# Performance work log

Measured on AMD Instinct MI355X. Metric: run time of the kernel, lower is better.

The kernel has to match this reference:

```python
import jax, jax.numpy as jnp
import numpy as np
import math

B, S, D = 4, 2048, 1024
NH = 8
DH = D // NH
EPS = 1e-6


def setup_inputs() -> dict:
    key = jax.random.key(0)
    k0, k1, k2, k3, k4, k5 = jax.random.split(key, 6)
    q = jax.random.normal(k0, (B, S, D), jnp.float32)
    k = jax.random.normal(k1, (B, S, D), jnp.float32)
    v = jax.random.normal(k2, (B, S, D), jnp.float32)
    # Gate Dense params. Original inits kernels to zeros; use small random
    # kernels so gates actually depend on the input.
    W_i = jax.random.normal(k3, (3 * D, NH), jnp.float32) * 0.02
    b_i = jax.random.normal(k4, (NH,), jnp.float32) * 0.1
    W_f = jax.random.normal(k5, (3 * D, NH), jnp.float32) * 0.02
    b_f = jnp.linspace(3.0, 6.0, NH, dtype=jnp.float32)  # bias_linspace_init(3,6)
    ln_w = jnp.ones((NH, DH), jnp.float32)  # MultiHeadLayerNorm weight (no bias)
    c_state = jnp.zeros((B, NH, DH, DH), jnp.float32)
    n_state = jnp.zeros((B, NH, DH, 1), jnp.float32)
    m_state = jnp.zeros((B, NH, 1, 1), jnp.float32)
    return {"q": q, "k": k, "v": v, "c_state": c_state, "n_state": n_state,
            "m_state": m_state, "W_i": W_i, "b_i": b_i, "W_f": W_f,
            "b_f": b_f, "ln_w": ln_w}


def _mlstm_forward(q, k, v, c_state, n_state, m_state, W_i, b_i, W_f, b_f, ln_w):
    Bq, Sq, Dq = q.shape
    nh = b_i.shape[0]
    dh = Dq // nh
    scale = 1.0 / math.sqrt(dh)

    qkv = jnp.concatenate([q, k, v], axis=-1)            # (B,S,3D)
    ig = (qkv @ W_i + b_i).transpose(0, 2, 1)            # (B,NH,S)
    fg = (qkv @ W_f + b_f).transpose(0, 2, 1)            # (B,NH,S)

    # Faithful 'weaving' reshape (no head transpose!)
    qh = q.reshape(Bq, nh, Sq, dh)
    kh = k.reshape(Bq, nh, Sq, dh)
    vh = v.reshape(Bq, nh, Sq, dh)

    # scan layout: time-major
    qs = qh.transpose(2, 0, 1, 3)                        # (S,B,NH,DH)
    ks_ = kh.transpose(2, 0, 1, 3)
    vs = vh.transpose(2, 0, 1, 3)
    igs = ig.transpose(2, 0, 1)[:, :, :, None, None]     # (S,B,NH,1,1)
    fgs = fg.transpose(2, 0, 1)[:, :, :, None, None]

    def step(carry, xs):
        c, n, m = carry
        qt, kt, vt, ft, it = xs
        qt = qt[:, :, None, :]                           # (B,NH,1,DH)
        kt = kt[..., None]                               # (B,NH,DH,1)
        vt = vt[:, :, None, :]                           # (B,NH,1,DH)
        log_f = jax.nn.log_sigmoid(ft)                   # (B,NH,1,1)
        m_new = jnp.maximum(log_f + m, it)
        f_act = jnp.exp(log_f + m - m_new)
        i_act = jnp.exp(it - m_new)
        k_sc = kt * scale
        c_new = f_act * c + i_act * (k_sc @ vt)          # (B,NH,DH,DH)
        n_new = f_act * n + i_act * k_sc                 # (B,NH,DH,1)
        h_num = qt @ c_new                               # (B,NH,1,DH)
        qn = qt @ n_new                                  # (B,NH,1,1)
        denom = jnp.maximum(jnp.abs(qn), jnp.exp(-m_new)) + EPS
        h = (h_num / denom).squeeze(axis=2)              # (B,NH,DH)
        return (c_new, n_new, m_new), h

    (c_f, n_f, m_f), out = jax.lax.scan(
        step, (c_state, n_state, m_state), (qs, ks_, vs, fgs, igs))
    h = out.transpose(1, 2, 0, 3)                        # (B,NH,S,DH)

    # MultiHeadLayerNorm over DH, per-head scale, no bias
    mu = h.mean(axis=-1, keepdims=True)
    var = h.var(axis=-1, keepdims=True)
    hn = (h - mu) * jax.lax.rsqrt(var + 1e-6) * ln_w[None, :, None, :]
    hn = hn.transpose(0, 2, 1, 3).reshape(Bq, Sq, Dq)
    return hn, c_f, n_f, m_f


def reference(q, k, v, c_state, n_state, m_state, W_i, b_i, W_f, b_f, ln_w):
    return _mlstm_forward(q, k, v, c_state, n_state, m_state,
                          W_i, b_i, W_f, b_f, ln_w)
```

## Files before the change

### kernel.cpp

```cpp
#include <hip/hip_runtime.h>
#include <math.h>

#define BB 4
#define SS 2048
#define DD 1024
#define NHD 8
#define DHD 128
#define NC 16
#define CL 128
#define SCALE 0.08838834764831845f

#define OFF_IG   0
#define OFF_LF   65536
#define OFF_B    131072
#define OFF_G    196608
#define OFF_E    262144
#define OFF_RM   327680
#define OFF_MIN  393216
#define OFF_SC   393728
#define OFF_UN   396288
#define OFF_NIN  461824
#define OFF_U    527360
#define OFF_KH   4721664
#define OFF_VT   8915968
#define OUT_C  8388608
#define OUT_N  8912896
#define OUT_M  8916992

typedef __attribute__((ext_vector_type(8))) _Float16 f16x8;
typedef __attribute__((ext_vector_type(4))) float f32x4;

__device__ __forceinline__ unsigned pk2h(float a, float b) {
  union { _Float16 h[2]; unsigned u; } f;
  f.h[0] = (_Float16)a; f.h[1] = (_Float16)b;
  return f.u;
}
__device__ __forceinline__ f16x8 mkfrag(float4 a, float4 c) {
  f16x8 f;
  f[0] = (_Float16)a.x; f[1] = (_Float16)a.y; f[2] = (_Float16)a.z; f[3] = (_Float16)a.w;
  f[4] = (_Float16)c.x; f[5] = (_Float16)c.y; f[6] = (_Float16)c.z; f[7] = (_Float16)c.w;
  return f;
}
__device__ __forceinline__ char* swp(char* base, int row, int byte) {
  return base + (((row << 8) + byte) ^ ((row & 7) << 4));
}

__global__ __launch_bounds__(256) void wtrans_kernel(const float* __restrict__ Wi,
                                                     const float* __restrict__ Wf,
                                                     _Float16* __restrict__ WT) {
  const int kk = blockIdx.x * 256 + threadIdx.x;
  float4 wa = *(const float4*)(Wi + (size_t)kk * 8);
  float4 wb = *(const float4*)(Wi + (size_t)kk * 8 + 4);
  float4 fa = *(const float4*)(Wf + (size_t)kk * 8);
  float4 fb = *(const float4*)(Wf + (size_t)kk * 8 + 4);
  WT[0 * 3072 + kk]  = (_Float16)wa.x; WT[1 * 3072 + kk]  = (_Float16)wa.y;
  WT[2 * 3072 + kk]  = (_Float16)wa.z; WT[3 * 3072 + kk]  = (_Float16)wa.w;
  WT[4 * 3072 + kk]  = (_Float16)wb.x; WT[5 * 3072 + kk]  = (_Float16)wb.y;
  WT[6 * 3072 + kk]  = (_Float16)wb.z; WT[7 * 3072 + kk]  = (_Float16)wb.w;
  WT[8 * 3072 + kk]  = (_Float16)fa.x; WT[9 * 3072 + kk]  = (_Float16)fa.y;
  WT[10 * 3072 + kk] = (_Float16)fa.z; WT[11 * 3072 + kk] = (_Float16)fa.w;
  WT[12 * 3072 + kk] = (_Float16)fb.x; WT[13 * 3072 + kk] = (_Float16)fb.y;
  WT[14 * 3072 + kk] = (_Float16)fb.z; WT[15 * 3072 + kk] = (_Float16)fb.w;
}

__global__ __launch_bounds__(512) void gates_kernel(
    const float* __restrict__ q, const float* __restrict__ k, const float* __restrict__ v,
    const _Float16* __restrict__ WT, const float* __restrict__ bi,
    const float* __restrict__ bfb,
    float* __restrict__ ig_ws, float* __restrict__ lf_ws,
    _Float16* __restrict__ kh) {
  __shared__ float red[8][256];
  const int tid = threadIdx.x, wid = tid >> 6, lane = tid & 63;
  const int g16 = lane >> 4, l15 = lane & 15;
  const int g0 = blockIdx.x * 16;
  const int b = g0 >> 11, t0 = g0 & (SS - 1);

  const size_t rowoff = (size_t)b * SS * DD + (size_t)(t0 + l15) * DD;
  const float* qr = q + rowoff;
  const float* kr = k + rowoff;
  const float* vr = v + rowoff;

  f32x4 acc = {0.f, 0.f, 0.f, 0.f};
  const int ks0 = wid * 12;
  #pragma unroll
  for (int grp = 0; grp < 3; ++grp) {
    const int s0 = ks0 + grp * 4;
    const int seg = s0 >> 5;
    const float* base = (seg == 0) ? qr : (seg == 1) ? kr : vr;
    const float* Ab = base + (s0 & 31) * 32 + g16 * 8;
    const _Float16* Bb = WT + l15 * 3072 + s0 * 32 + g16 * 8;
    float4 a[4], c[4]; f16x8 bfr[4];
    #pragma unroll
    for (int j = 0; j < 4; ++j) {
      a[j]   = *(const float4*)(Ab + j * 32);
      c[j]   = *(const float4*)(Ab + j * 32 + 4);
      bfr[j] = *(const f16x8*)(Bb + j * 32);
    }
    if (seg == 1) {
      const int coff = (s0 & 31) * 32 + g16 * 8;
      #pragma unroll
      for (int j = 0; j < 4; ++j)
        *(f16x8*)(kh + rowoff + coff + j * 32) = mkfrag(a[j], c[j]);
    }
    #pragma unroll
    for (int j = 0; j < 4; ++j)
      acc = __builtin_amdgcn_mfma_f32_16x16x32_f16(mkfrag(a[j], c[j]), bfr[j], acc, 0, 0, 0);
  }
  #pragma unroll
  for (int r = 0; r < 4; ++r) red[wid][(g16 * 4 + r) * 16 + l15] = acc[r];
  __syncthreads();

  if (tid < 256) {
    float s = 0.f;
    #pragma unroll
    for (int w = 0; w < 8; ++w) s += red[w][tid];
    const int row = tid >> 4, gate = tid & 15;
    const int t = t0 + row;
    if (gate < 8) {
      ig_ws[(size_t)(b * NHD + gate) * SS + t] = s + bi[gate];
    } else {
      float ft = s + bfb[gate - 8];
      float lf = fminf(ft, 0.f) - log1pf(expf(-fabsf(ft)));
      lf_ws[(size_t)(b * NHD + gate - 8) * SS + t] = lf;
    }
  }
}

__global__ __launch_bounds__(128) void prep1_kernel(float* __restrict__ ws) {
  const int g  = blockIdx.x & 15;
  const int bh = blockIdx.x >> 4;
  const int s  = threadIdx.x;
  __shared__ float sh[128];
  __shared__ float bc1;
  const int t = g * CL + s;
  float lfv = ws[OFF_LF + (size_t)bh * SS + t];
  float iv  = ws[OFF_IG + (size_t)bh * SS + t];
  float v = lfv;
  sh[s] = v; __syncthreads();
  for (int off = 1; off < 128; off <<= 1) {
    float tv = (s >= off) ? sh[s - off] : 0.f;
    __syncthreads();
    v += tv; sh[s] = v; __syncthreads();
  }
  float Bv = v;
  float Gv = iv - Bv;
  v = Gv; sh[s] = v; __syncthreads();
  for (int off = 1; off < 128; off <<= 1) {
    float tv = (s >= off) ? sh[s - off] : -3.0e38f;
    __syncthreads();
    v = fmaxf(v, tv); sh[s] = v; __syncthreads();
  }
  float Rv = v;
  if (s == 127) bc1 = Rv;
  __syncthreads();
  float mxG = bc1;
  ws[OFF_B  + (size_t)bh * SS + t] = Bv;
  ws[OFF_G  + (size_t)bh * SS + t] = Gv;
  ws[OFF_RM + (size_t)bh * SS + t] = Rv;
  ws[OFF_E  + (size_t)bh * SS + t] = expf(Gv - mxG);
}

__global__ __launch_bounds__(64) void prep2_kernel(float* __restrict__ ws,
                                                   const float* __restrict__ m0,
                                                   float* __restrict__ out) {
  const int bh = blockIdx.x;
  if (threadIdx.x != 0) return;
  const float m0v = m0[bh];
  float m_run = m0v, LFtot = 0.f;
  float mina[NC], mxga[NC], lfsa[NC];
  #pragma unroll
  for (int g = 0; g < NC; ++g) {
    float Bend = ws[OFF_B  + (size_t)bh * SS + g * CL + 127];
    float mxG  = ws[OFF_RM + (size_t)bh * SS + g * CL + 127];
    ws[OFF_MIN + bh * NC + g] = m_run;
    mina[g] = m_run; mxga[g] = mxG; lfsa[g] = LFtot;
    m_run = Bend + fmaxf(m_run, mxG);
    LFtot += Bend;
  }
  out[OUT_M + bh] = m_run;
  float* sc = ws + OFF_SC + bh * 80;
  float S = -3.0e38f;
  #pragma unroll
  for (int g = 0; g < NC; ++g) {
    float r_g = lfsa[g] - mina[g];
    sc[g]      = expf(S + r_g);
    sc[20 + g] = expf(m0v + lfsa[g] - mina[g]);
    float s_g = mxga[g] - lfsa[g];
    float Sn = fmaxf(S, s_g);
    sc[40 + g] = expf(S - Sn);
    sc[60 + g] = expf(s_g - Sn);
    S = Sn;
  }
  sc[16] = expf(S + LFtot - m_run);
  sc[36] = expf(m0v + LFtot - m_run);
}

__global__ __launch_bounds__(256, 2) void u_kernel(const float* __restrict__ k,
                                                   const float* __restrict__ v,
                                                   float* __restrict__ ws) {
  extern __shared__ char smem[];
  char* Kt = smem;
  char* Vt = smem + 32768;

  const int tid = threadIdx.x;
  const int wid = tid >> 6;
  const int lane = tid & 63;
  const int g16 = lane >> 4;
  const int l15 = lane & 15;
  const int g  = blockIdx.x & 15;
  const int bh = blockIdx.x >> 4;
  const int b = bh >> 3, hh = bh & 7;
  const size_t headoff = (size_t)b * SS * DD + (size_t)hh * SS * DHD;
  const float* kb = k + headoff + (size_t)g * CL * DHD;
  const float* vb = v + headoff + (size_t)g * CL * DHD;
  const float* E  = ws + OFF_E + (size_t)bh * SS + g * CL;

  #pragma unroll 4
  for (int it = 0; it < 16; ++it) {
    const int idx = (it << 8) + tid;
    const int c  = idx & 127;
    const int r0 = (idx >> 7) << 2;
    float e0 = E[r0] * SCALE, e1 = E[r0 + 1] * SCALE,
          e2 = E[r0 + 2] * SCALE, e3 = E[r0 + 3] * SCALE;
    float a0 = kb[(size_t)r0 * DHD + c] * e0;
    float a1 = kb[(size_t)(r0 + 1) * DHD + c] * e1;
    float a2 = kb[(size_t)(r0 + 2) * DHD + c] * e2;
    float a3 = kb[(size_t)(r0 + 3) * DHD + c] * e3;
    *(uint2*)swp(Kt, c, r0 * 2) = make_uint2(pk2h(a0, a1), pk2h(a2, a3));
    float b0 = vb[(size_t)r0 * DHD + c];
    float b1 = vb[(size_t)(r0 + 1) * DHD + c];
    float b2 = vb[(size_t)(r0 + 2) * DHD + c];
    float b3 = vb[(size_t)(r0 + 3) * DHD + c];
    *(uint2*)swp(Vt, c, r0 * 2) = make_uint2(pk2h(b0, b1), pk2h(b2, b3));
  }
  __syncthreads();

  _Float16* VTg = (_Float16*)(ws + OFF_VT) + (size_t)(bh * NC + g) * 16384;
  #pragma unroll
  for (int it2 = 0; it2 < 8; ++it2) {
    const int ci = (it2 << 8) + tid;
    const int j = ci >> 4, rp = ci & 15;
    f16x8 x = *(f16x8*)swp(Vt, j, rp * 16);
    *(f16x8*)(VTg + j * 128 + rp * 8) = x;
  }

  if (tid < 128) {
    float s = 0.f;
    #pragma unroll
    for (int r8 = 0; r8 < 16; ++r8) {
      f16x8 x = *(f16x8*)swp(Kt, tid, r8 * 16);
      s += (float)x[0] + (float)x[1] + (float)x[2] + (float)x[3]
         + (float)x[4] + (float)x[5] + (float)x[6] + (float)x[7];
    }
    ws[OFF_UN + (size_t)(bh * NC + g) * DHD + tid] = s;
  }

  _Float16* UTb = (_Float16*)(ws + OFF_U) + (size_t)(bh * NC + g) * 16384;
  const int it0 = wid * 2;
  #pragma unroll 1
  for (int jt = 0; jt < 8; ++jt) {
    f32x4 a0 = {0.f, 0.f, 0.f, 0.f}, a1 = {0.f, 0.f, 0.f, 0.f};
    #pragma unroll
    for (int kst = 0; kst < 4; ++kst) {
      const int byte = (kst * 32 + g16 * 8) * 2;
      f16x8 av = *(f16x8*)swp(Vt, jt * 16 + l15, byte);
      f16x8 b0 = *(f16x8*)swp(Kt, it0 * 16 + l15, byte);
      f16x8 b1 = *(f16x8*)swp(Kt, (it0 + 1) * 16 + l15, byte);
      a0 = __builtin_amdgcn_mfma_f32_16x16x32_f16(av, b0, a0, 0, 0, 0);
      a1 = __builtin_amdgcn_mfma_f32_16x16x32_f16(av, b1, a1, 0, 0, 0);
    }
    #pragma unroll
    for (int reg = 0; reg < 4; ++reg) {
      UTb[(size_t)(jt * 16 + g16 * 4 + reg) * DHD + it0 * 16 + l15] = (_Float16)a0[reg];
      UTb[(size_t)(jt * 16 + g16 * 4 + reg) * DHD + (it0 + 1) * 16 + l15] = (_Float16)a1[reg];
    }
  }
}

__global__ __launch_bounds__(256) void cprefix_kernel(const float* __restrict__ c0,
                                                      float* __restrict__ ws,
                                                      float* __restrict__ out) {
  const int bh = blockIdx.x >> 6;
  const int elem = ((blockIdx.x & 63) << 8) + threadIdx.x;
  const int j = elem >> 7, i = elem & 127;
  const float* sc = ws + OFF_SC + bh * 80;
  float c0v = c0[(size_t)bh * 16384 + i * 128 + j];
  _Float16* Ub = (_Float16*)(ws + OFF_U) + (size_t)bh * NC * 16384 + elem;
  float uv[16];
  #pragma unroll
  for (int g = 0; g < NC; ++g) uv[g] = (float)Ub[(size_t)g * 16384];
  float P = 0.f;
  _Float16 cin[16];
  #pragma unroll
  for (int g = 0; g < NC; ++g) {
    cin[g] = (_Float16)(sc[g] * P + sc[20 + g] * c0v);
    P = sc[40 + g] * P + sc[60 + g] * uv[g];
  }
  #pragma unroll
  for (int g = 0; g < NC; ++g) Ub[(size_t)g * 16384] = cin[g];
  out[OUT_C + (size_t)bh * 16384 + i * 128 + j] = sc[16] * P + sc[36] * c0v;
}

__global__ __launch_bounds__(128) void nprefix_kernel(const float* __restrict__ n0,
                                                      float* __restrict__ ws,
                                                      float* __restrict__ out) {
  const int bh = blockIdx.x;
  const int i = threadIdx.x;
  const float* sc = ws + OFF_SC + bh * 80;
  float n0v = n0[bh * DHD + i];
  const float* Ub = ws + OFF_UN + (size_t)bh * NC * DHD + i;
  float* Nb = ws + OFF_NIN + (size_t)bh * NC * DHD + i;
  float uv[16];
  #pragma unroll
  for (int g = 0; g < NC; ++g) uv[g] = Ub[g * DHD];
  float P = 0.f;
  float nin[16];
  #pragma unroll
  for (int g = 0; g < NC; ++g) {
    nin[g] = sc[g] * P + sc[20 + g] * n0v;
    P = sc[40 + g] * P + sc[60 + g] * uv[g];
  }
  #pragma unroll
  for (int g = 0; g < NC; ++g) Nb[g * DHD] = nin[g];
  out[OUT_N + bh * DHD + i] = sc[16] * P + sc[36] * n0v;
}

__global__ __launch_bounds__(512, 4) void intra_kernel(
    const float* __restrict__ q, const _Float16* __restrict__ kh,
    const float* __restrict__ lnw, float* __restrict__ ws, float* __restrict__ out) {
  const int tid = threadIdx.x;
  const int wid = tid >> 6;
  const int lane = tid & 63;
  const int g16 = lane >> 4;
  const int l15 = lane & 15;
  const int g = blockIdx.x & 15;
  const int bh = blockIdx.x >> 4;
  const int b = bh >> 3, hh = bh & 7;
  const int t0 = g * CL;
  const int st = wid;
  const int stmax = st | 1;
  const int srow = st * 16 + l15;

  const size_t headoff = (size_t)b * SS * DD + (size_t)hh * SS * DHD;
  const float* qb = q + headoff;
  const _Float16* khb = kh + headoff;
  const _Float16* CinT = (const _Float16*)(ws + OFF_U) + (size_t)(bh * NC + g) * 16384;
  const _Float16* VTb  = (const _Float16*)(ws + OFF_VT) + (size_t)(bh * NC + g) * 16384;
  const float* ninb = ws + OFF_NIN + (size_t)(bh * NC + g) * DHD;
  const float* Gb   = ws + OFF_G + (size_t)bh * SS + t0;

  const float m_in = ws[OFF_MIN + bh * NC + g];
  const float Rv_l = ws[OFF_RM + (size_t)bh * SS + t0 + srow];
  const float Bs_l = ws[OFF_B  + (size_t)bh * SS + t0 + srow];
  const float Ms_l = fmaxf(m_in, Rv_l);
  const float al_l = __expf(m_in - Ms_l);

  f16x8 qf[4];
  float qn2 = 0.f;
  {
    const float* qrow = qb + (size_t)(t0 + srow) * DHD + g16 * 8;
    float4 a[4], c[4];
    #pragma unroll
    for (int kst = 0; kst < 4; ++kst) {
      a[kst] = *(const float4*)(qrow + kst * 32);
      c[kst] = *(const float4*)(qrow + kst * 32 + 4);
    }
    float4 n0v[4], n1v[4];
    #pragma unroll
    for (int kst = 0; kst < 4; ++kst) {
      n0v[kst] = *(const float4*)(ninb + kst * 32 + g16 * 8);
      n1v[kst] = *(const float4*)(ninb + kst * 32 + g16 * 8 + 4);
    }
    #pragma unroll
    for (int kst = 0; kst < 4; ++kst) {
      qf[kst] = mkfrag(a[kst], c[kst]);
      qn2 += a[kst].x * n0v[kst].x + a[kst].y * n0v[kst].y
           + a[kst].z * n0v[kst].z + a[kst].w * n0v[kst].w
           + c[kst].x * n1v[kst].x + c[kst].y * n1v[kst].y
           + c[kst].z * n1v[kst].z + c[kst].w * n1v[kst].w;
    }
    qn2 += __shfl_xor(qn2, 16); qn2 += __shfl_xor(qn2, 32);
  }

  f32x4 acc[8];
  #pragma unroll
  for (int jtp = 0; jtp < 4; ++jtp) {
    f16x8 bfr[8];
    #pragma unroll
    for (int jj = 0; jj < 2; ++jj)
      #pragma unroll
      for (int kst = 0; kst < 4; ++kst)
        bfr[jj * 4 + kst] = *(const f16x8*)(CinT +
            (size_t)((jtp * 2 + jj) * 16 + l15) * DHD + kst * 32 + g16 * 8);
    #pragma unroll
    for (int jj = 0; jj < 2; ++jj) {
      f32x4 a0 = {0.f, 0.f, 0.f, 0.f};
      #pragma unroll
      for (int kst = 0; kst < 4; ++kst)
        a0 = __builtin_amdgcn_mfma_f32_16x16x32_f16(qf[kst], bfr[jj * 4 + kst], a0, 0, 0, 0);
      acc[jtp * 2 + jj] = a0;
    }
  }
  {
    float av[4];
    #pragma unroll
    for (int reg = 0; reg < 4; ++reg) av[reg] = __shfl(al_l, g16 * 4 + reg);
    #pragma unroll
    for (int jt = 0; jt < 8; ++jt) {
      acc[jt][0] *= av[0]; acc[jt][1] *= av[1];
      acc[jt][2] *= av[2]; acc[jt][3] *= av[3];
    }
  }

  unsigned pk[8][2];
  float qns = 0.f;
  #pragma unroll
  for (int rtb = 0; rtb < 4; ++rtb) {
    const int rt0 = 2 * rtb;
    if (rt0 <= stmax) {
      const _Float16* kr0 = khb + (size_t)(t0 + rt0 * 16 + l15) * DHD + g16 * 8;
      f16x8 kf[8];
      #pragma unroll
      for (int kst = 0; kst < 4; ++kst) {
        kf[kst]     = *(const f16x8*)(kr0 + kst * 32);
        kf[4 + kst] = *(const f16x8*)(kr0 + 16 * DHD + kst * 32);
      }
      float4 Gq0 = *(const float4*)(Gb + rt0 * 16 + g16 * 4);
      float4 Gq1 = *(const float4*)(Gb + (rt0 + 1) * 16 + g16 * 4);
      f32x4 sa0 = {0.f, 0.f, 0.f, 0.f}, sa1 = {0.f, 0.f, 0.f, 0.f};
      #pragma unroll
      for (int kst = 0; kst < 4; ++kst) {
        sa0 = __builtin_amdgcn_mfma_f32_16x16x32_f16(kf[kst], qf[kst], sa0, 0, 0, 0);
        sa1 = __builtin_amdgcn_mfma_f32_16x16x32_f16(kf[4 + kst], qf[kst], sa1, 0, 0, 0);
      }
      const float* G0 = (const float*)&Gq0;
      const float* G1 = (const float*)&Gq1;
      float vr0[4], vr1[4];
      #pragma unroll
      for (int rr = 0; rr < 4; ++rr) {
        const int r0i = rt0 * 16 + g16 * 4 + rr;
        const int r1i = r0i + 16;
        float w0 = (r0i <= srow) ? __expf(G0[rr] - Ms_l) * SCALE : 0.f;
        float w1 = (r1i <= srow) ? __expf(G1[rr] - Ms_l) * SCALE : 0.f;
        vr0[rr] = sa0[rr] * w0;
        vr1[rr] = sa1[rr] * w1;
      }
      qns += vr0[0] + vr0[1] + vr0[2] + vr0[3] + vr1[0] + vr1[1] + vr1[2] + vr1[3];
      pk[rt0][0]     = pk2h(vr0[0], vr0[1]);
      pk[rt0][1]     = pk2h(vr0[2], vr0[3]);
      pk[rt0 + 1][0] = pk2h(vr1[0], vr1[1]);
      pk[rt0 + 1][1] = pk2h(vr1[2], vr1[3]);
    }
  }
  qns += __shfl_xor(qns, 16); qns += __shfl_xor(qns, 32);
  const float pfull = qns + al_l * qn2;

  const int kmax = (stmax + 1) >> 1;
  const int srcb = ((g16 & 1) << 5) + l15;
  const bool upper = g16 >= 2;
  #pragma unroll
  for (int kst = 0; kst < 4; ++kst) {
    if (kst < kmax) {
      f16x8 vf[8];
      #pragma unroll
      for (int jt = 0; jt < 8; ++jt)
        vf[jt] = *(const f16x8*)(VTb + (size_t)(jt * 16 + l15) * DHD + kst * 32 + g16 * 8);
      unsigned l0 = __shfl(pk[2 * kst][0], srcb);
      unsigned l1 = __shfl(pk[2 * kst][1], srcb);
      unsigned l2 = __shfl(pk[2 * kst][0], srcb + 16);
      unsigned l3 = __shfl(pk[2 * kst][1], srcb + 16);
      unsigned h0 = __shfl(pk[2 * kst + 1][0], srcb);
      unsigned h1 = __shfl(pk[2 * kst + 1][1], srcb);
      unsigned h2 = __shfl(pk[2 * kst + 1][0], srcb + 16);
      unsigned h3 = __shfl(pk[2 * kst + 1][1], srcb + 16);
      union { unsigned u[4]; f16x8 h; } pa;
      pa.u[0] = upper ? h0 : l0;
      pa.u[1] = upper ? h1 : l1;
      pa.u[2] = upper ? h2 : l2;
      pa.u[3] = upper ? h3 : l3;
      #pragma unroll
      for (int jt = 0; jt < 8; ++jt)
        acc[jt] = __builtin_amdgcn_mfma_f32_16x16x32_f16(pa.h, vf[jt], acc[jt], 0, 0, 0);
    }
  }

  const float* lw = lnw + hh * DHD;
  float lwv[8];
  #pragma unroll
  for (int jt = 0; jt < 8; ++jt) lwv[jt] = lw[jt * 16 + l15];

  const int s0 = st * 16 + g16 * 4;
  #pragma unroll
  for (int reg = 0; reg < 4; ++reg) {
    float qn_r = __shfl(pfull, g16 * 4 + reg);
    float B_r  = __shfl(Bs_l,  g16 * 4 + reg);
    float M_r  = __shfl(Ms_l,  g16 * 4 + reg);
    float den = fmaxf(fabsf(qn_r), __expf(-(B_r + M_r))) + 1e-6f;
    float inv = 1.0f / den;
    float mp = 0.f, sp = 0.f;
    float hv[8];
    #pragma unroll
    for (int jt = 0; jt < 8; ++jt) {
      float h = acc[jt][reg] * inv;
      hv[jt] = h;
      mp += h; sp += h * h;
    }
    mp += __shfl_xor(mp, 1); sp += __shfl_xor(sp, 1);
    mp += __shfl_xor(mp, 2); sp += __shfl_xor(sp, 2);
    mp += __shfl_xor(mp, 4); sp += __shfl_xor(sp, 4);
    mp += __shfl_xor(mp, 8); sp += __shfl_xor(sp, 8);
    float mu = mp * (1.f / 128.f);
    float var = fmaxf(sp * (1.f / 128.f) - mu * mu, 0.f);
    float rstd = rsqrtf(var + 1e-6f);
    float* orow = out + (size_t)(b * SS + t0 + s0 + reg) * DD + hh * DHD;
    #pragma unroll
    for (int jt = 0; jt < 8; ++jt)
      orow[jt * 16 + l15] = (hv[jt] - mu) * rstd * lwv[jt];
  }
}

extern "C" void kernel_launch(void* const* d_in, const int* in_sizes, int n_in,
                              void* d_out, int out_size, void* d_ws, size_t ws_size,
                              hipStream_t stream) {
  const float* q   = (const float*)d_in[0];
  const float* k   = (const float*)d_in[1];
  const float* v   = (const float*)d_in[2];
  const float* c0  = (const float*)d_in[3];
  const float* n0  = (const float*)d_in[4];
  const float* m0  = (const float*)d_in[5];
  const float* Wi  = (const float*)d_in[6];
  const float* bi  = (const float*)d_in[7];
  const float* Wf  = (const float*)d_in[8];
  const float* bf  = (const float*)d_in[9];
  const float* lnw = (const float*)d_in[10];
  float* out = (float*)d_out;
  float* ws  = (float*)d_ws;

  _Float16* WT = (_Float16*)(ws + OFF_U);
  _Float16* kh = (_Float16*)(ws + OFF_KH);

  wtrans_kernel<<<12, 256, 0, stream>>>(Wi, Wf, WT);
  gates_kernel<<<BB * SS / 16, 512, 0, stream>>>(q, k, v, WT, bi, bf,
                                                 ws + OFF_IG, ws + OFF_LF, kh);
  prep1_kernel<<<BB * NHD * NC, 128, 0, stream>>>(ws);
  prep2_kernel<<<BB * NHD, 64, 0, stream>>>(ws, m0, out);
  u_kernel<<<BB * NHD * NC, 256, 65536, stream>>>(k, v, ws);
  cprefix_kernel<<<BB * NHD * 64, 256, 0, stream>>>(c0, ws, out);
  nprefix_kernel<<<BB * NHD, 128, 0, stream>>>(n0, ws, out);
  intra_kernel<<<BB * NHD * NC, 512, 0, stream>>>(q, kh, lnw, ws, out);
}
```

Before: 120.2 us.

## Double wavefronts per block in gates and intra kernels by splitting work

The gates kernel now runs 16 waves per block, each covering half as many K-steps, and the shared-memory reduction sums 16 partials instead of 8. The intra kernel splits each 16-row strip's 128 output columns across two waves. Row statistics for the layer norm are combined through shared memory with a block barrier. This raises parallelism and lowers per-wave register pressure, since intra was limited to 512 blocks. The cost is more redundant q and score work per wave, extra synchronisation, and launch_bounds(1024,4) that may be hard to satisfy.

After: 139.4 us. +16.0%, slower.

```diff
diff --git a/kernel.cpp b/kernel.cpp
--- a/kernel.cpp
+++ b/kernel.cpp
@@ -63,13 +63,13 @@
   WT[14 * 3072 + kk] = (_Float16)fb.z; WT[15 * 3072 + kk] = (_Float16)fb.w;
 }
 
-__global__ __launch_bounds__(512) void gates_kernel(
+__global__ __launch_bounds__(1024) void gates_kernel(
     const float* __restrict__ q, const float* __restrict__ k, const float* __restrict__ v,
     const _Float16* __restrict__ WT, const float* __restrict__ bi,
     const float* __restrict__ bfb,
     float* __restrict__ ig_ws, float* __restrict__ lf_ws,
     _Float16* __restrict__ kh) {
-  __shared__ float red[8][256];
+  __shared__ float red[16][256];
   const int tid = threadIdx.x, wid = tid >> 6, lane = tid & 63;
   const int g16 = lane >> 4, l15 = lane & 15;
   const int g0 = blockIdx.x * 16;
@@ -81,17 +81,17 @@
   const float* vr = v + rowoff;
 
   f32x4 acc = {0.f, 0.f, 0.f, 0.f};
-  const int ks0 = wid * 12;
+  const int ks0 = wid * 6;
   #pragma unroll
   for (int grp = 0; grp < 3; ++grp) {
-    const int s0 = ks0 + grp * 4;
+    const int s0 = ks0 + grp * 2;
     const int seg = s0 >> 5;
     const float* base = (seg == 0) ? qr : (seg == 1) ? kr : vr;
     const float* Ab = base + (s0 & 31) * 32 + g16 * 8;
     const _Float16* Bb = WT + l15 * 3072 + s0 * 32 + g16 * 8;
-    float4 a[4], c[4]; f16x8 bfr[4];
-    #pragma unroll
-    for (int j = 0; j < 4; ++j) {
+    float4 a[2], c[2]; f16x8 bfr[2];
+    #pragma unroll
+    for (int j = 0; j < 2; ++j) {
       a[j]   = *(const float4*)(Ab + j * 32);
       c[j]   = *(const float4*)(Ab + j * 32 + 4);
       bfr[j] = *(const f16x8*)(Bb + j * 32);
@@ -99,11 +99,11 @@
     if (seg == 1) {
       const int coff = (s0 & 31) * 32 + g16 * 8;
       #pragma unroll
-      for (int j = 0; j < 4; ++j)
+      for (int j = 0; j < 2; ++j)
         *(f16x8*)(kh + rowoff + coff + j * 32) = mkfrag(a[j], c[j]);
     }
     #pragma unroll
-    for (int j = 0; j < 4; ++j)
+    for (int j = 0; j < 2; ++j)
       acc = __builtin_amdgcn_mfma_f32_16x16x32_f16(mkfrag(a[j], c[j]), bfr[j], acc, 0, 0, 0);
   }
   #pragma unroll
@@ -113,7 +113,7 @@
   if (tid < 256) {
     float s = 0.f;
     #pragma unroll
-    for (int w = 0; w < 8; ++w) s += red[w][tid];
+    for (int w = 0; w < 16; ++w) s += red[w][tid];
     const int row = tid >> 4, gate = tid & 15;
     const int t = t0 + row;
     if (gate < 8) {
@@ -325,11 +325,15 @@
   out[OUT_N + bh * DHD + i] = sc[16] * P + sc[36] * n0v;
 }
 
-__global__ __launch_bounds__(512, 4) void intra_kernel(
+__global__ __launch_bounds__(1024, 4) void intra_kernel(
     const float* __restrict__ q, const _Float16* __restrict__ kh,
     const float* __restrict__ lnw, float* __restrict__ ws, float* __restrict__ out) {
+  __shared__ float redmp[16][16];
+  __shared__ float redsp[16][16];
   const int tid = threadIdx.x;
-  const int wid = tid >> 6;
+  const int w = tid >> 6;
+  const int st = w >> 1;
+  const int jh = w & 1;
   const int lane = tid & 63;
   const int g16 = lane >> 4;
   const int l15 = lane & 15;
@@ -337,9 +341,9 @@
   const int bh = blockIdx.x >> 4;
   const int b = bh >> 3, hh = bh & 7;
   const int t0 = g * CL;
-  const int st = wid;
   const int stmax = st | 1;
   const int srow = st * 16 + l15;
+  const int jbase = jh * 4;
 
   const size_t headoff = (size_t)b * SS * DD + (size_t)hh * SS * DHD;
   const float* qb = q + headoff;
@@ -382,16 +386,16 @@
     qn2 += __shfl_xor(qn2, 16); qn2 += __shfl_xor(qn2, 32);
   }
 
-  f32x4 acc[8];
-  #pragma unroll
-  for (int jtp = 0; jtp < 4; ++jtp) {
+  f32x4 acc[4];
+  #pragma unroll
+  for (int jtp = 0; jtp < 2; ++jtp) {
     f16x8 bfr[8];
     #pragma unroll
     for (int jj = 0; jj < 2; ++jj)
       #pragma unroll
       for (int kst = 0; kst < 4; ++kst)
         bfr[jj * 4 + kst] = *(const f16x8*)(CinT +
-            (size_t)((jtp * 2 + jj) * 16 + l15) * DHD + kst * 32 + g16 * 8);
+            (size_t)((jbase + jtp * 2 + jj) * 16 + l15) * DHD + kst * 32 + g16 * 8);
     #pragma unroll
     for (int jj = 0; jj < 2; ++jj) {
       f32x4 a0 = {0.f, 0.f, 0.f, 0.f};
@@ -406,7 +410,7 @@
     #pragma unroll
     for (int reg = 0; reg < 4; ++reg) av[reg] = __shfl(al_l, g16 * 4 + reg);
     #pragma unroll
-    for (int jt = 0; jt < 8; ++jt) {
+    for (int jt = 0; jt < 4; ++jt) {
       acc[jt][0] *= av[0]; acc[jt][1] *= av[1];
       acc[jt][2] *= av[2]; acc[jt][3] *= av[3];
     }
@@ -461,10 +465,10 @@
   #pragma unroll
   for (int kst = 0; kst < 4; ++kst) {
     if (kst < kmax) {
-      f16x8 vf[8];
-      #pragma unroll
-      for (int jt = 0; jt < 8; ++jt)
-        vf[jt] = *(const f16x8*)(VTb + (size_t)(jt * 16 + l15) * DHD + kst * 32 + g16 * 8);
+      f16x8 vf[4];
+      #pragma unroll
+      for (int jt = 0; jt < 4; ++jt)
+        vf[jt] = *(const f16x8*)(VTb + (size_t)((jbase + jt) * 16 + l15) * DHD + kst * 32 + g16 * 8);
       unsigned l0 = __shfl(pk[2 * kst][0], srcb);
       unsigned l1 = __shfl(pk[2 * kst][1], srcb);
       unsigned l2 = __shfl(pk[2 * kst][0], srcb + 16);
@@ -479,17 +483,11 @@
       pa.u[2] = upper ? h2 : l2;
       pa.u[3] = upper ? h3 : l3;
       #pragma unroll
-      for (int jt = 0; jt < 8; ++jt)
+      for (int jt = 0; jt < 4; ++jt)
         acc[jt] = __builtin_amdgcn_mfma_f32_16x16x32_f16(pa.h, vf[jt], acc[jt], 0, 0, 0);
     }
   }
 
-  const float* lw = lnw + hh * DHD;
-  float lwv[8];
-  #pragma unroll
-  for (int jt = 0; jt < 8; ++jt) lwv[jt] = lw[jt * 16 + l15];
-
-  const int s0 = st * 16 + g16 * 4;
   #pragma unroll
   for (int reg = 0; reg < 4; ++reg) {
     float qn_r = __shfl(pfull, g16 * 4 + reg);
@@ -498,24 +496,40 @@
     float den = fmaxf(fabsf(qn_r), __expf(-(B_r + M_r))) + 1e-6f;
     float inv = 1.0f / den;
     float mp = 0.f, sp = 0.f;
-    float hv[8];
-    #pragma unroll
-    for (int jt = 0; jt < 8; ++jt) {
+    #pragma unroll
+    for (int jt = 0; jt < 4; ++jt) {
       float h = acc[jt][reg] * inv;
-      hv[jt] = h;
+      acc[jt][reg] = h;
       mp += h; sp += h * h;
     }
     mp += __shfl_xor(mp, 1); sp += __shfl_xor(sp, 1);
     mp += __shfl_xor(mp, 2); sp += __shfl_xor(sp, 2);
     mp += __shfl_xor(mp, 4); sp += __shfl_xor(sp, 4);
     mp += __shfl_xor(mp, 8); sp += __shfl_xor(sp, 8);
-    float mu = mp * (1.f / 128.f);
-    float var = fmaxf(sp * (1.f / 128.f) - mu * mu, 0.f);
+    if (l15 == 0) {
+      redmp[w][g16 * 4 + reg] = mp;
+      redsp[w][g16 * 4 + reg] = sp;
+    }
+  }
+  __syncthreads();
+
+  const float* lw = lnw + hh * DHD;
+  float lwv[4];
+  #pragma unroll
+  for (int jt = 0; jt < 4; ++jt) lwv[jt] = lw[(jbase + jt) * 16 + l15];
+
+  const int s0 = st * 16 + g16 * 4;
+  #pragma unroll
+  for (int reg = 0; reg < 4; ++reg) {
+    float mpf = redmp[w][g16 * 4 + reg] + redmp[w ^ 1][g16 * 4 + reg];
+    float spf = redsp[w][g16 * 4 + reg] + redsp[w ^ 1][g16 * 4 + reg];
+    float mu = mpf * (1.f / 128.f);
+    float var = fmaxf(spf * (1.f / 128.f) - mu * mu, 0.f);
     float rstd = rsqrtf(var + 1e-6f);
     float* orow = out + (size_t)(b * SS + t0 + s0 + reg) * DD + hh * DHD;
     #pragma unroll
-    for (int jt = 0; jt < 8; ++jt)
-      orow[jt * 16 + l15] = (hv[jt] - mu) * rstd * lwv[jt];
+    for (int jt = 0; jt < 4; ++jt)
+      orow[(jbase + jt) * 16 + l15] = (acc[jt][reg] - mu) * rstd * lwv[jt];
   }
 }
 
@@ -540,12 +554,12 @@
   _Float16* kh = (_Float16*)(ws + OFF_KH);
 
   wtrans_kernel<<<12, 256, 0, stream>>>(Wi, Wf, WT);
-  gates_kernel<<<BB * SS / 16, 512, 0, stream>>>(q, k, v, WT, bi, bf,
-                                                 ws + OFF_IG, ws + OFF_LF, kh);
+  gates_kernel<<<BB * SS / 16, 1024, 0, stream>>>(q, k, v, WT, bi, bf,
+                                                  ws + OFF_IG, ws + OFF_LF, kh);
   prep1_kernel<<<BB * NHD * NC, 128, 0, stream>>>(ws);
   prep2_kernel<<<BB * NHD, 64, 0, stream>>>(ws, m0, out);
   u_kernel<<<BB * NHD * NC, 256, 65536, stream>>>(k, v, ws);
   cprefix_kernel<<<BB * NHD * 64, 256, 0, stream>>>(c0, ws, out);
   nprefix_kernel<<<BB * NHD, 128, 0, stream>>>(n0, ws, out);
-  intra_kernel<<<BB * NHD * NC, 512, 0, stream>>>(q, kh, lnw, ws, out);
-}
+  intra_kernel<<<BB * NHD * NC, 1024, 0, stream>>>(q, kh, lnw, ws, out);
+}
```

## Split gate GEMM K-dimension across two blocks and widen u_kernel to 512 threads

Applied to the files above, without the earlier changes.

The gates kernel now splits the 3072-long reduction into two halves handled by separate blocks, doubling the grid. Each half writes partial sums to its own workspace buffer. The bias add and log-sigmoid move into prep1, which sums the two partials. u_kernel runs 512 threads per block with each wave owning one output tile instead of two, which adds parallelism per block. The cost is extra workspace traffic for the partial gate buffers, and u_kernel loses its explicit occupancy hint.

Result: faster. 113.0 us (median of 2 runs) (-6.0%).

```diff
diff --git a/kernel.cpp b/kernel.cpp
--- a/kernel.cpp
+++ b/kernel.cpp
@@ -23,6 +23,8 @@
 #define OFF_U    527360
 #define OFF_KH   4721664
 #define OFF_VT   8915968
+#define OFF_IG2  13110272
+#define OFF_LF2  13175808
 #define OUT_C  8388608
 #define OUT_N  8912896
 #define OUT_M  8916992
@@ -65,14 +67,14 @@
 
 __global__ __launch_bounds__(512) void gates_kernel(
     const float* __restrict__ q, const float* __restrict__ k, const float* __restrict__ v,
-    const _Float16* __restrict__ WT, const float* __restrict__ bi,
-    const float* __restrict__ bfb,
-    float* __restrict__ ig_ws, float* __restrict__ lf_ws,
+    const _Float16* __restrict__ WT, float* __restrict__ ws,
     _Float16* __restrict__ kh) {
   __shared__ float red[8][256];
   const int tid = threadIdx.x, wid = tid >> 6, lane = tid & 63;
   const int g16 = lane >> 4, l15 = lane & 15;
-  const int g0 = blockIdx.x * 16;
+  const int khalf = blockIdx.x & 1;
+  const int rb = blockIdx.x >> 1;
+  const int g0 = rb * 16;
   const int b = g0 >> 11, t0 = g0 & (SS - 1);
 
   const size_t rowoff = (size_t)b * SS * DD + (size_t)(t0 + l15) * DD;
@@ -81,17 +83,17 @@
   const float* vr = v + rowoff;
 
   f32x4 acc = {0.f, 0.f, 0.f, 0.f};
-  const int ks0 = wid * 12;
+  const int ks0 = khalf * 48 + wid * 6;
   #pragma unroll
   for (int grp = 0; grp < 3; ++grp) {
-    const int s0 = ks0 + grp * 4;
+    const int s0 = ks0 + grp * 2;
     const int seg = s0 >> 5;
     const float* base = (seg == 0) ? qr : (seg == 1) ? kr : vr;
     const float* Ab = base + (s0 & 31) * 32 + g16 * 8;
     const _Float16* Bb = WT + l15 * 3072 + s0 * 32 + g16 * 8;
-    float4 a[4], c[4]; f16x8 bfr[4];
-    #pragma unroll
-    for (int j = 0; j < 4; ++j) {
+    float4 a[2], c[2]; f16x8 bfr[2];
+    #pragma unroll
+    for (int j = 0; j < 2; ++j) {
       a[j]   = *(const float4*)(Ab + j * 32);
       c[j]   = *(const float4*)(Ab + j * 32 + 4);
       bfr[j] = *(const f16x8*)(Bb + j * 32);
@@ -99,11 +101,11 @@
     if (seg == 1) {
       const int coff = (s0 & 31) * 32 + g16 * 8;
       #pragma unroll
-      for (int j = 0; j < 4; ++j)
+      for (int j = 0; j < 2; ++j)
         *(f16x8*)(kh + rowoff + coff + j * 32) = mkfrag(a[j], c[j]);
     }
     #pragma unroll
-    for (int j = 0; j < 4; ++j)
+    for (int j = 0; j < 2; ++j)
       acc = __builtin_amdgcn_mfma_f32_16x16x32_f16(mkfrag(a[j], c[j]), bfr[j], acc, 0, 0, 0);
   }
   #pragma unroll
@@ -116,37 +118,39 @@
     for (int w = 0; w < 8; ++w) s += red[w][tid];
     const int row = tid >> 4, gate = tid & 15;
     const int t = t0 + row;
-    if (gate < 8) {
-      ig_ws[(size_t)(b * NHD + gate) * SS + t] = s + bi[gate];
-    } else {
-      float ft = s + bfb[gate - 8];
-      float lf = fminf(ft, 0.f) - log1pf(expf(-fabsf(ft)));
-      lf_ws[(size_t)(b * NHD + gate - 8) * SS + t] = lf;
-    }
-  }
-}
-
-__global__ __launch_bounds__(128) void prep1_kernel(float* __restrict__ ws) {
+    float* igb = ws + (khalf ? OFF_IG2 : OFF_IG);
+    float* lfb = ws + (khalf ? OFF_LF2 : OFF_LF);
+    if (gate < 8) igb[(size_t)(b * NHD + gate) * SS + t] = s;
+    else          lfb[(size_t)(b * NHD + gate - 8) * SS + t] = s;
+  }
+}
+
+__global__ __launch_bounds__(128) void prep1_kernel(float* __restrict__ ws,
+                                                    const float* __restrict__ bi,
+                                                    const float* __restrict__ bfb) {
   const int g  = blockIdx.x & 15;
   const int bh = blockIdx.x >> 4;
+  const int hh = bh & 7;
   const int s  = threadIdx.x;
   __shared__ float sh[128];
   __shared__ float bc1;
   const int t = g * CL + s;
-  float lfv = ws[OFF_LF + (size_t)bh * SS + t];
-  float iv  = ws[OFF_IG + (size_t)bh * SS + t];
+  const size_t off = (size_t)bh * SS + t;
+  float ft  = ws[OFF_LF + off] + ws[OFF_LF2 + off] + bfb[hh];
+  float lfv = fminf(ft, 0.f) - log1pf(expf(-fabsf(ft)));
+  float iv  = ws[OFF_IG + off] + ws[OFF_IG2 + off] + bi[hh];
   float v = lfv;
   sh[s] = v; __syncthreads();
-  for (int off = 1; off < 128; off <<= 1) {
-    float tv = (s >= off) ? sh[s - off] : 0.f;
+  for (int off2 = 1; off2 < 128; off2 <<= 1) {
+    float tv = (s >= off2) ? sh[s - off2] : 0.f;
     __syncthreads();
     v += tv; sh[s] = v; __syncthreads();
   }
   float Bv = v;
   float Gv = iv - Bv;
   v = Gv; sh[s] = v; __syncthreads();
-  for (int off = 1; off < 128; off <<= 1) {
-    float tv = (s >= off) ? sh[s - off] : -3.0e38f;
+  for (int off2 = 1; off2 < 128; off2 <<= 1) {
+    float tv = (s >= off2) ? sh[s - off2] : -3.0e38f;
     __syncthreads();
     v = fmaxf(v, tv); sh[s] = v; __syncthreads();
   }
@@ -154,10 +158,10 @@
   if (s == 127) bc1 = Rv;
   __syncthreads();
   float mxG = bc1;
-  ws[OFF_B  + (size_t)bh * SS + t] = Bv;
-  ws[OFF_G  + (size_t)bh * SS + t] = Gv;
-  ws[OFF_RM + (size_t)bh * SS + t] = Rv;
-  ws[OFF_E  + (size_t)bh * SS + t] = expf(Gv - mxG);
+  ws[OFF_B  + off] = Bv;
+  ws[OFF_G  + off] = Gv;
+  ws[OFF_RM + off] = Rv;
+  ws[OFF_E  + off] = expf(Gv - mxG);
 }
 
 __global__ __launch_bounds__(64) void prep2_kernel(float* __restrict__ ws,
@@ -195,9 +199,9 @@
   sc[36] = expf(m0v + LFtot - m_run);
 }
 
-__global__ __launch_bounds__(256, 2) void u_kernel(const float* __restrict__ k,
-                                                   const float* __restrict__ v,
-                                                   float* __restrict__ ws) {
+__global__ __launch_bounds__(512) void u_kernel(const float* __restrict__ k,
+                                                const float* __restrict__ v,
+                                                float* __restrict__ ws) {
   extern __shared__ char smem[];
   char* Kt = smem;
   char* Vt = smem + 32768;
@@ -216,8 +220,8 @@
   const float* E  = ws + OFF_E + (size_t)bh * SS + g * CL;
 
   #pragma unroll 4
-  for (int it = 0; it < 16; ++it) {
-    const int idx = (it << 8) + tid;
+  for (int it = 0; it < 8; ++it) {
+    const int idx = (it << 9) + tid;
     const int c  = idx & 127;
     const int r0 = (idx >> 7) << 2;
     float e0 = E[r0] * SCALE, e1 = E[r0 + 1] * SCALE,
@@ -237,8 +241,8 @@
 
   _Float16* VTg = (_Float16*)(ws + OFF_VT) + (size_t)(bh * NC + g) * 16384;
   #pragma unroll
-  for (int it2 = 0; it2 < 8; ++it2) {
-    const int ci = (it2 << 8) + tid;
+  for (int it2 = 0; it2 < 4; ++it2) {
+    const int ci = (it2 << 9) + tid;
     const int j = ci >> 4, rp = ci & 15;
     f16x8 x = *(f16x8*)swp(Vt, j, rp * 16);
     *(f16x8*)(VTg + j * 128 + rp * 8) = x;
@@ -256,24 +260,20 @@
   }
 
   _Float16* UTb = (_Float16*)(ws + OFF_U) + (size_t)(bh * NC + g) * 16384;
-  const int it0 = wid * 2;
+  const int it0 = wid;
   #pragma unroll 1
   for (int jt = 0; jt < 8; ++jt) {
-    f32x4 a0 = {0.f, 0.f, 0.f, 0.f}, a1 = {0.f, 0.f, 0.f, 0.f};
+    f32x4 a0 = {0.f, 0.f, 0.f, 0.f};
     #pragma unroll
     for (int kst = 0; kst < 4; ++kst) {
       const int byte = (kst * 32 + g16 * 8) * 2;
       f16x8 av = *(f16x8*)swp(Vt, jt * 16 + l15, byte);
       f16x8 b0 = *(f16x8*)swp(Kt, it0 * 16 + l15, byte);
-      f16x8 b1 = *(f16x8*)swp(Kt, (it0 + 1) * 16 + l15, byte);
       a0 = __builtin_amdgcn_mfma_f32_16x16x32_f16(av, b0, a0, 0, 0, 0);
-      a1 = __builtin_amdgcn_mfma_f32_16x16x32_f16(av, b1, a1, 0, 0, 0);
-    }
-    #pragma unroll
-    for (int reg = 0; reg < 4; ++reg) {
+    }
+    #pragma unroll
+    for (int reg = 0; reg < 4; ++reg)
       UTb[(size_t)(jt * 16 + g16 * 4 + reg) * DHD + it0 * 16 + l15] = (_Float16)a0[reg];
-      UTb[(size_t)(jt * 16 + g16 * 4 + reg) * DHD + (it0 + 1) * 16 + l15] = (_Float16)a1[reg];
-    }
   }
 }
 
@@ -540,11 +540,10 @@
   _Float16* kh = (_Float16*)(ws + OFF_KH);
 
   wtrans_kernel<<<12, 256, 0, stream>>>(Wi, Wf, WT);
-  gates_kernel<<<BB * SS / 16, 512, 0, stream>>>(q, k, v, WT, bi, bf,
-                                                 ws + OFF_IG, ws + OFF_LF, kh);
-  prep1_kernel<<<BB * NHD * NC, 128, 0, stream>>>(ws);
+  gates_kernel<<<BB * SS / 16 * 2, 512, 0, stream>>>(q, k, v, WT, ws, kh);
+  prep1_kernel<<<BB * NHD * NC, 128, 0, stream>>>(ws, bi, bf);
   prep2_kernel<<<BB * NHD, 64, 0, stream>>>(ws, m0, out);
-  u_kernel<<<BB * NHD * NC, 256, 65536, stream>>>(k, v, ws);
+  u_kernel<<<BB * NHD * NC, 512, 65536, stream>>>(k, v, ws);
   cprefix_kernel<<<BB * NHD * 64, 256, 0, stream>>>(c0, ws, out);
   nprefix_kernel<<<BB * NHD, 128, 0, stream>>>(n0, ws, out);
   intra_kernel<<<BB * NHD * NC, 512, 0, stream>>>(q, kh, lnw, ws, out);
```
